# Kernel optimization log

Hardware: AMD Instinct MI355X
Metric: run time of the kernel (lower is better)

## Reference

```python
import jax, jax.numpy as jnp
import numpy as np

N_NODES = 100000
N_EDGES = 1600000
IN_DIM, HID_DIM, OUT_DIM = 128, 64, 64


def setup_inputs() -> dict:
    key = jax.random.key(0)
    ks = jax.random.split(key, 12)
    x = jax.random.normal(ks[0], (N_NODES, IN_DIM), dtype=jnp.float32)
    src = jax.random.randint(ks[1], (N_EDGES,), 0, N_NODES, dtype=jnp.int32)
    dst = jax.random.randint(ks[2], (N_EDGES,), 0, N_NODES, dtype=jnp.int32)
    def glorot(k, shape):
        lim = float(np.sqrt(6.0 / (shape[0] + shape[1])))
        return jax.random.uniform(k, shape, jnp.float32, -lim, lim)
    W0 = glorot(ks[3], (IN_DIM, HID_DIM)); b0 = jnp.zeros((HID_DIM,), jnp.float32)
    W1 = glorot(ks[4], (HID_DIM, HID_DIM)); b1 = jnp.zeros((HID_DIM,), jnp.float32)
    W2 = glorot(ks[5], (HID_DIM, OUT_DIM)); b2 = jnp.zeros((OUT_DIM,), jnp.float32)
    Wl = glorot(ks[6], (OUT_DIM, OUT_DIM)); bl = jnp.zeros((OUT_DIM,), jnp.float32)
    return {"x": x, "src": src, "dst": dst,
            "W0": W0, "b0": b0, "W1": W1, "b1": b1,
            "W2": W2, "b2": b2, "Wl": Wl, "bl": bl}


def _graph_conv(x, src, dst, W, b, inv_sqrt_out, inv_sqrt_in):
    # DGL GraphConv, norm='both': D_out^{-1/2} then XW, SpMM aggregate, D_in^{-1/2}, +bias
    h = x * inv_sqrt_out[:, None]          # [N, d_in]
    h = h @ W                               # [N, d_out] (project first: d_in >= d_out)
    agg = jax.ops.segment_sum(h[src], dst, num_segments=N_NODES)  # gather+scatter over edges
    return agg * inv_sqrt_in[:, None] + b


def reference(x, src, dst, W0, b0, W1, b1, W2, b2, Wl, bl):
    ones_e = jnp.ones((N_EDGES,), jnp.float32)
    deg_out = jnp.clip(jax.ops.segment_sum(ones_e, src, num_segments=N_NODES), 1.0)
    deg_in = jnp.clip(jax.ops.segment_sum(ones_e, dst, num_segments=N_NODES), 1.0)
    inv_out = jax.lax.rsqrt(deg_out)
    inv_in = jax.lax.rsqrt(deg_in)
    h = jax.nn.elu(_graph_conv(x, src, dst, W0, b0, inv_out, inv_in))
    h = jax.nn.elu(_graph_conv(h, src, dst, W1, b1, inv_out, inv_in))
    h = _graph_conv(h, src, dst, W2, b2, inv_out, inv_in)
    return jax.nn.elu(h) @ Wl + bl
```

## Files before the change

### kernel.cpp

```cpp
#include <hip/hip_runtime.h>
#include <hip/hip_fp16.h>
#include <cstdint>
#include <cstddef>


#define WG 256
static constexpr int NCHUNK = 512;
static constexpr int RW_SH  = 7;
static constexpr int RWID   = 1 << RW_SH;
static constexpr int BPRO   = 32000;
static constexpr int NRO    = 4;
static constexpr int NCO    = 64;

typedef _Float16 half8 __attribute__((ext_vector_type(8)));
typedef _Float16 half2v __attribute__((ext_vector_type(2)));
typedef float f32x4 __attribute__((ext_vector_type(4)));

__device__ __forceinline__ int block_scan_excl(int v, int tid, int* sd, int& total) {
  sd[tid] = v;
  __syncthreads();
  for (int off = 1; off < 256; off <<= 1) {
    int t = (tid >= off) ? sd[tid - off] : 0;
    __syncthreads();
    sd[tid] += t;
    __syncthreads();
  }
  int incl = sd[tid];
  total = sd[255];
  __syncthreads();
  return incl - v;
}

__global__ __launch_bounds__(WG) void setup1_kernel(const int* __restrict__ src,
                                                    const int* __restrict__ dst,
                                                    int* __restrict__ cntA,
                                                    int* __restrict__ slab,
                                                    const float* __restrict__ W0,
                                                    const float* __restrict__ W1,
                                                    const float* __restrict__ W2,
                                                    const float* __restrict__ Wl,
                                                    _Float16* __restrict__ T0,
                                                    _Float16* __restrict__ T1,
                                                    _Float16* __restrict__ T2,
                                                    _Float16* __restrict__ Tl,
                                                    int NR, int N, int E, int EPC, int EPCO) {
  __shared__ int smem[BPRO / 2];
  const int b = blockIdx.x, tid = threadIdx.x;

  if (b < NCHUNK) {
    int* cnt = smem;
    for (int i = tid; i < NR; i += WG) cnt[i] = 0;
    __syncthreads();
    const int base = b * EPC;
    const int nv4 = EPC >> 2;
    const int4* d4 = (const int4*)(dst + base);
    for (int i = tid; i < nv4; i += WG) {
      const int e = base + (i << 2);
      if (e + 3 < E) {
        const int4 v = d4[i];
        atomicAdd(&cnt[v.x >> RW_SH], 1);
        atomicAdd(&cnt[v.y >> RW_SH], 1);
        atomicAdd(&cnt[v.z >> RW_SH], 1);
        atomicAdd(&cnt[v.w >> RW_SH], 1);
      } else {
        for (int j = 0; j < 4; ++j) {
          const int ee = e + j;
          if (ee < E) atomicAdd(&cnt[dst[ee] >> RW_SH], 1);
        }
      }
    }
    __syncthreads();
    for (int i = tid; i < NR; i += WG) cntA[i * NCHUNK + b] = cnt[i];
    return;
  }

  if (b < NCHUNK + NRO * NCO) {
    int* h = smem;
    const int bb = b - NCHUNK;
    const int rr = bb / NCO, cc = bb % NCO;
    for (int i = tid; i < (BPRO >> 3); i += WG) ((int4*)h)[i] = make_int4(0, 0, 0, 0);
    __syncthreads();
    const int lo = rr * BPRO;
    const int base = cc * EPCO;
    const int nv4 = EPCO >> 2;
    const int4* s4 = (const int4*)(src + base);
    for (int i = tid; i < nv4; i += WG) {
      const int e = base + (i << 2);
      if (e + 3 < E) {
        const int4 v = s4[i];
        unsigned x;
        x = (unsigned)(v.x - lo); if (x < (unsigned)BPRO) atomicAdd((unsigned*)&h[x >> 1], 1u << ((x & 1) << 4));
        x = (unsigned)(v.y - lo); if (x < (unsigned)BPRO) atomicAdd((unsigned*)&h[x >> 1], 1u << ((x & 1) << 4));
        x = (unsigned)(v.z - lo); if (x < (unsigned)BPRO) atomicAdd((unsigned*)&h[x >> 1], 1u << ((x & 1) << 4));
        x = (unsigned)(v.w - lo); if (x < (unsigned)BPRO) atomicAdd((unsigned*)&h[x >> 1], 1u << ((x & 1) << 4));
      } else {
        for (int j = 0; j < 4; ++j) {
          const int ee = e + j;
          if (ee < E) {
            const unsigned x = (unsigned)(src[ee] - lo);
            if (x < (unsigned)BPRO) atomicAdd((unsigned*)&h[x >> 1], 1u << ((x & 1) << 4));
          }
        }
      }
    }
    __syncthreads();
    const int NW = N >> 1;
    const int wbase = lo >> 1;
    int* srow = slab + (size_t)cc * NW;
    for (int i = tid; i < (BPRO >> 3); i += WG) {
      const int wg = wbase + (i << 2);
      if (wg + 3 < NW) {
        ((int4*)(srow + wg))[0] = ((const int4*)h)[i];
      } else {
        for (int j = 0; j < 4; ++j)
          if (wg + j < NW) srow[wg + j] = h[(i << 2) + j];
      }
    }
    return;
  }

  const float* W; _Float16* T; int K;
  switch (b - (NCHUNK + NRO * NCO)) {
    case 0: W = W0; T = T0; K = 128; break;
    case 1: W = W1; T = T1; K = 64; break;
    case 2: W = W2; T = T2; K = 64; break;
    default: W = Wl; T = Tl; K = 64; break;
  }
  for (int i = tid; i < K * 64; i += WG) {
    const int k = i >> 6, c = i & 63;
    T[c * K + k] = (_Float16)W[i];
  }
}

__global__ __launch_bounds__(WG) void setup2_kernel(const int* __restrict__ cntA,
                                                    int* __restrict__ base_rel,
                                                    int* __restrict__ cntR,
                                                    const int* __restrict__ slab,
                                                    float* __restrict__ invo,
                                                    int NR, int N) {
  __shared__ int sd[256];
  const int b = blockIdx.x, tid = threadIdx.x;

  if (b < NR) {
    const int row = b * NCHUNK;
    int t0, t1;
    const int v0 = cntA[row + tid];
    const int e0 = block_scan_excl(v0, tid, sd, t0);
    base_rel[row + tid] = e0;
    const int v1 = cntA[row + 256 + tid];
    const int e1 = block_scan_excl(v1, tid, sd, t1);
    base_rel[row + 256 + tid] = t0 + e1;
    if (tid == 0) cntR[b] = t0 + t1;
    return;
  }

  const int NW = N >> 1;
  const int i = (b - NR) * WG + tid;
  if (i >= NW) return;
  unsigned s = 0;
#pragma unroll
  for (int c = 0; c < NCO; ++c) s += (unsigned)slab[(size_t)c * NW + i];
  int d0 = (int)(s & 0xffffu); if (d0 < 1) d0 = 1;
  int d1 = (int)(s >> 16);     if (d1 < 1) d1 = 1;
  *(float2*)(invo + 2 * i) = make_float2(rsqrtf((float)d0), rsqrtf((float)d1));
}

template <int K, bool F16IN>
__device__ __forceinline__ void gemm_conv_body(int bid, const void* __restrict__ inv_,
                                               const _Float16* __restrict__ WT,
                                               const float* __restrict__ invo,
                                               _Float16* __restrict__ hP, int N) {
  const int tid = threadIdx.x;
  const int w = tid >> 6, l = tid & 63;
  const int rowA = bid * 64 + w * 16 + (l & 15);
  const int ar = (rowA < N) ? rowA : (N - 1);
  const int g8 = (l >> 4) * 8;

  f32x4 acc[4];
#pragma unroll
  for (int t = 0; t < 4; ++t) acc[t] = (f32x4){0.f, 0.f, 0.f, 0.f};

#pragma unroll
  for (int s = 0; s < K / 32; ++s) {
    const int kb = s * 32 + g8;
    half8 a;
    if constexpr (F16IN) {
      a = *(const half8*)((const _Float16*)inv_ + (size_t)ar * K + kb);
    } else {
      const float* in = (const float*)inv_;
      const float4 f0 = *(const float4*)(in + (size_t)ar * K + kb);
      const float4 f1 = *(const float4*)(in + (size_t)ar * K + kb + 4);
      a[0] = (_Float16)f0.x; a[1] = (_Float16)f0.y; a[2] = (_Float16)f0.z; a[3] = (_Float16)f0.w;
      a[4] = (_Float16)f1.x; a[5] = (_Float16)f1.y; a[6] = (_Float16)f1.z; a[7] = (_Float16)f1.w;
    }
#pragma unroll
    for (int t = 0; t < 4; ++t) {
      const half8 b = *(const half8*)(WT + (size_t)(16 * t + (l & 15)) * K + kb);
      acc[t] = __builtin_amdgcn_mfma_f32_16x16x32_f16(a, b, acc[t], 0, 0, 0);
    }
  }

  const int rbase = bid * 64 + w * 16 + (l >> 4) * 4;
#pragma unroll
  for (int r = 0; r < 4; ++r) {
    const int row = rbase + r;
    if (row < N) {
      const float sc = invo[row];
#pragma unroll
      for (int t = 0; t < 4; ++t)
        hP[(size_t)row * 64 + 16 * t + (l & 15)] = (_Float16)(acc[t][r] * sc);
    }
  }
}

__global__ __launch_bounds__(WG) void range_gemm0_kernel(const int* __restrict__ cntR,
                                                         int* __restrict__ rangeStart,
                                                         int* __restrict__ rptr,
                                                         const float* __restrict__ x,
                                                         const _Float16* __restrict__ WT0,
                                                         const float* __restrict__ invo,
                                                         _Float16* __restrict__ hP,
                                                         int NR, int N, int E) {
  __shared__ int sd[256];
  const int b = blockIdx.x, tid = threadIdx.x;
  if (b == 0) {
    int carry = 0;
    for (int base = 0; base < NR; base += 256) {
      const int idx = base + tid;
      const int v = (idx < NR) ? cntR[idx] : 0;
      int tot;
      const int e = block_scan_excl(v, tid, sd, tot);
      if (idx < NR) rangeStart[idx] = carry + e;
      carry += tot;
    }
    if (tid == 0) { rangeStart[NR] = E; rptr[N] = E; }
    return;
  }
  gemm_conv_body<128, false>(b - 1, x, WT0, invo, hP, N);
}

__global__ __launch_bounds__(WG) void bucket_kernel(const int* __restrict__ src,
                                                    const int* __restrict__ dst,
                                                    const int* __restrict__ base_rel,
                                                    const int* __restrict__ rangeStart,
                                                    int* __restrict__ bucket,
                                                    int NR, int E, int EPC) {
  __shared__ int cur[1024];
  const int c = blockIdx.x, tid = threadIdx.x;
  for (int i = tid; i < NR; i += WG) cur[i] = rangeStart[i] + base_rel[i * NCHUNK + c];
  __syncthreads();
  const int base = c * EPC;
  const int nv4 = EPC >> 2;
  const int4* s4 = (const int4*)(src + base);
  const int4* d4 = (const int4*)(dst + base);
  for (int i = tid; i < nv4; i += WG) {
    const int e = base + (i << 2);
    if (e + 3 < E) {
      const int4 sv = s4[i];
      const int4 dv = d4[i];
      int p;
      p = atomicAdd(&cur[dv.x >> RW_SH], 1); bucket[p] = (sv.x << RW_SH) | (dv.x & (RWID - 1));
      p = atomicAdd(&cur[dv.y >> RW_SH], 1); bucket[p] = (sv.y << RW_SH) | (dv.y & (RWID - 1));
      p = atomicAdd(&cur[dv.z >> RW_SH], 1); bucket[p] = (sv.z << RW_SH) | (dv.z & (RWID - 1));
      p = atomicAdd(&cur[dv.w >> RW_SH], 1); bucket[p] = (sv.w << RW_SH) | (dv.w & (RWID - 1));
    } else {
      for (int j = 0; j < 4; ++j) {
        const int ee = e + j;
        if (ee < E) {
          const int s = src[ee], d = dst[ee];
          const int p = atomicAdd(&cur[d >> RW_SH], 1);
          bucket[p] = (s << RW_SH) | (d & (RWID - 1));
        }
      }
    }
  }
}

__global__ __launch_bounds__(WG) void csr_kernel(const int* __restrict__ bucket,
                                                 const int* __restrict__ rangeStart,
                                                 int* __restrict__ rptr,
                                                 float* __restrict__ invi,
                                                 int* __restrict__ esrc, int N) {
  __shared__ int hist[RWID], sd[256];
  const int r = blockIdx.x, tid = threadIdx.x;
  const int s0 = rangeStart[r], s1 = rangeStart[r + 1];
  if (tid < RWID) hist[tid] = 0;
  __syncthreads();
  for (int e = s0 + tid; e < s1; e += WG) atomicAdd(&hist[bucket[e] & (RWID - 1)], 1);
  __syncthreads();
  const int v = (tid < RWID) ? hist[tid] : 0;
  int tot;
  const int excl = block_scan_excl(v, tid, sd, tot);
  const int node = (r << RW_SH) + tid;
  if (tid < RWID && node < N) {
    rptr[node] = s0 + excl;
    invi[node] = rsqrtf((float)((v < 1) ? 1 : v));
  }
  if (tid < RWID) hist[tid] = s0 + excl;
  __syncthreads();
  for (int e = s0 + tid; e < s1; e += WG) {
    const int pk = bucket[e];
    const int p = atomicAdd(&hist[pk & (RWID - 1)], 1);
    esrc[p] = pk >> RW_SH;
  }
}

template <int K, bool F16IN>
__global__ __launch_bounds__(256) void gemm_conv_mfma(const void* __restrict__ inv_,
                                                      const _Float16* __restrict__ WT,
                                                      const float* __restrict__ invo,
                                                      _Float16* __restrict__ hP, int N) {
  gemm_conv_body<K, F16IN>(blockIdx.x, inv_, WT, invo, hP, N);
}

__global__ __launch_bounds__(256) void gemm_head_mfma(const _Float16* __restrict__ in,
                                                      const _Float16* __restrict__ WT,
                                                      const float* __restrict__ bias,
                                                      float* __restrict__ out, int N) {
  constexpr int K = 64;
  const int tid = threadIdx.x;
  const int w = tid >> 6, l = tid & 63;
  const int rowA = blockIdx.x * 64 + w * 16 + (l & 15);
  const int ar = (rowA < N) ? rowA : (N - 1);
  const int g8 = (l >> 4) * 8;

  f32x4 acc[4];
#pragma unroll
  for (int t = 0; t < 4; ++t) acc[t] = (f32x4){0.f, 0.f, 0.f, 0.f};

#pragma unroll
  for (int s = 0; s < K / 32; ++s) {
    const int kb = s * 32 + g8;
    const half8 a = *(const half8*)(in + (size_t)ar * K + kb);
#pragma unroll
    for (int t = 0; t < 4; ++t) {
      const half8 b = *(const half8*)(WT + (size_t)(16 * t + (l & 15)) * K + kb);
      acc[t] = __builtin_amdgcn_mfma_f32_16x16x32_f16(a, b, acc[t], 0, 0, 0);
    }
  }

  const int rbase = blockIdx.x * 64 + w * 16 + (l >> 4) * 4;
#pragma unroll
  for (int r = 0; r < 4; ++r) {
    const int row = rbase + r;
    if (row < N) {
#pragma unroll
      for (int t = 0; t < 4; ++t) {
        const int c = 16 * t + (l & 15);
        out[(size_t)row * 64 + c] = acc[t][r] + bias[c];
      }
    }
  }
}

__global__ __launch_bounds__(256) void agg_kernel(const _Float16* __restrict__ hp,
                                                  const int* __restrict__ rptr,
                                                  const int* __restrict__ esrc,
                                                  const float* __restrict__ invin,
                                                  const float* __restrict__ bias,
                                                  _Float16* __restrict__ out, int N,
                                                  int apply_elu) {
  const int w = (blockIdx.x * 256 + threadIdx.x) >> 6;
  const int lane = threadIdx.x & 63;
  const int g = lane >> 3;
  const int f8 = lane & 7;
  if (w >= N) return;
  const int e0 = rptr[w];
  const int e1 = rptr[w + 1];
  const int f = f8 * 8 + g;
  const float vi = invin[w];
  const float bv = bias[f];

  float acc[8];
#pragma unroll
  for (int k = 0; k < 8; ++k) acc[k] = 0.f;

  int e = e0;
  for (; e + 16 <= e1; e += 16) {
    const int sA = esrc[e + g];
    const int sB = esrc[e + 8 + g];
    const half8 hA8 = *(const half8*)(hp + (size_t)sA * 64 + f8 * 8);
    const half8 hB8 = *(const half8*)(hp + (size_t)sB * 64 + f8 * 8);
#if __has_builtin(__builtin_amdgcn_fdot2)
    const half2v one2 = {(_Float16)1.0f, (_Float16)1.0f};
#pragma unroll
    for (int k = 0; k < 8; ++k) {
      half2v p; p[0] = hA8[k]; p[1] = hB8[k];
      acc[k] = __builtin_amdgcn_fdot2(p, one2, acc[k], false);
    }
#else
#pragma unroll
    for (int k = 0; k < 8; ++k) acc[k] += (float)hA8[k] + (float)hB8[k];
#endif
  }
  for (; e + 8 <= e1; e += 8) {
    const int s = esrc[e + g];
    const half8 hv = *(const half8*)(hp + (size_t)s * 64 + f8 * 8);
#pragma unroll
    for (int k = 0; k < 8; ++k) acc[k] += (float)hv[k];
  }
  if (e < e1) {
    const int rem = e1 - e;
    int idx = e + g; if (idx > e1 - 1) idx = e1 - 1;
    const int s = esrc[idx];
    const half8 hv = *(const half8*)(hp + (size_t)s * 64 + f8 * 8);
    const float m = (g < rem) ? 1.f : 0.f;
#pragma unroll
    for (int k = 0; k < 8; ++k) acc[k] = fmaf(m, (float)hv[k], acc[k]);
  }

  const bool gb0 = (g & 1) != 0;
  const float s0 = gb0 ? acc[0] : acc[1];
  const float s1 = gb0 ? acc[2] : acc[3];
  const float s2 = gb0 ? acc[4] : acc[5];
  const float s3 = gb0 ? acc[6] : acc[7];
  const float k0 = (gb0 ? acc[1] : acc[0]) + __shfl_xor(s0, 8);
  const float k1 = (gb0 ? acc[3] : acc[2]) + __shfl_xor(s1, 8);
  const float k2 = (gb0 ? acc[5] : acc[4]) + __shfl_xor(s2, 8);
  const float k3 = (gb0 ? acc[7] : acc[6]) + __shfl_xor(s3, 8);
  const bool gb1 = (g & 2) != 0;
  const float t0 = gb1 ? k0 : k1;
  const float t1 = gb1 ? k2 : k3;
  const float m0 = (gb1 ? k1 : k0) + __shfl_xor(t0, 16);
  const float m1 = (gb1 ? k3 : k2) + __shfl_xor(t1, 16);
  const bool gb2 = (g & 4) != 0;
  const float u0 = gb2 ? m0 : m1;
  float v = (gb2 ? m1 : m0) + __shfl_xor(u0, 32);

  v = v * vi + bv;
  if (apply_elu) v = (v > 0.f) ? v : (__expf(v) - 1.0f);
  out[(size_t)w * 64 + f] = (_Float16)v;
}

extern "C" void kernel_launch(void* const* d_in, const int* in_sizes, int n_in,
                              void* d_out, int out_size, void* d_ws, size_t ws_size,
                              hipStream_t stream) {
  const float* x  = (const float*)d_in[0];
  const int*   src = (const int*)d_in[1];
  const int*   dst = (const int*)d_in[2];
  const float* W0 = (const float*)d_in[3];
  const float* b0 = (const float*)d_in[4];
  const float* W1 = (const float*)d_in[5];
  const float* b1 = (const float*)d_in[6];
  const float* W2 = (const float*)d_in[7];
  const float* b2 = (const float*)d_in[8];
  const float* Wl = (const float*)d_in[9];
  const float* bl = (const float*)d_in[10];

  const int N = in_sizes[0] / 128;
  const int E = in_sizes[1];
  const int NR = (N + RWID - 1) >> RW_SH;
  const int EPC = (((E + NCHUNK - 1) / NCHUNK) + 3) & ~3;
  const int EPCO = (((E + NCO - 1) / NCO) + 3) & ~3;

  int* wsp = (int*)d_ws;
  size_t off = 0;
  auto alloc = [&](size_t n) -> int* {
    int* p = wsp + off;
    off += (n + 63) & ~(size_t)63;
    return p;
  };
  float*    invo       = (float*)alloc(N);
  float*    invi       = (float*)alloc(N);
  int*      rptr       = alloc((size_t)N + 1);
  int*      esrc       = alloc(E);
  int*      cntA       = alloc((size_t)NR * NCHUNK);
  int*      base_rel   = alloc((size_t)NR * NCHUNK);
  int*      cntR       = alloc(NR);
  int*      rangeStart = alloc((size_t)NR + 1);
  int*      bucket     = alloc(E);
  int*      slab       = alloc((size_t)NCO * (N >> 1));
  _Float16* hP         = (_Float16*)alloc((size_t)N * 32);
  _Float16* hA         = (_Float16*)alloc((size_t)N * 32);
  _Float16* WT0        = (_Float16*)alloc(64 * 128 / 2);
  _Float16* WT1        = (_Float16*)alloc(64 * 64 / 2);
  _Float16* WT2        = (_Float16*)alloc(64 * 64 / 2);
  _Float16* WTl        = (_Float16*)alloc(64 * 64 / 2);
  (void)ws_size; (void)n_in; (void)out_size;

  const int gAgg = (N + 3) / 4;
  const int gGemm = (N + 63) / 64;
  const int gInvo = ((N >> 1) + WG - 1) / WG;

  setup1_kernel<<<NCHUNK + NRO * NCO + 4, WG, 0, stream>>>(
      src, dst, cntA, slab, W0, W1, W2, Wl, WT0, WT1, WT2, WTl, NR, N, E, EPC, EPCO);
  setup2_kernel<<<NR + gInvo, WG, 0, stream>>>(cntA, base_rel, cntR, slab, invo, NR, N);
  range_gemm0_kernel<<<1 + gGemm, WG, 0, stream>>>(cntR, rangeStart, rptr, x, WT0, invo, hP, NR, N, E);
  bucket_kernel<<<NCHUNK, WG, 0, stream>>>(src, dst, base_rel, rangeStart, bucket, NR, E, EPC);
  csr_kernel<<<NR, WG, 0, stream>>>(bucket, rangeStart, rptr, invi, esrc, N);

  agg_kernel<<<gAgg, 256, 0, stream>>>(hP, rptr, esrc, invi, b0, hA, N, 1);
  gemm_conv_mfma<64, true><<<gGemm, 256, 0, stream>>>(hA, WT1, invo, hP, N);
  agg_kernel<<<gAgg, 256, 0, stream>>>(hP, rptr, esrc, invi, b1, hA, N, 1);
  gemm_conv_mfma<64, true><<<gGemm, 256, 0, stream>>>(hA, WT2, invo, hP, N);
  agg_kernel<<<gAgg, 256, 0, stream>>>(hP, rptr, esrc, invi, b2, hA, N, 1);
  gemm_head_mfma<<<gGemm, 256, 0, stream>>>(hA, WTl, bl, (float*)d_out, N);
}
```

Baseline: 240.8 us.

## Fold range scan into setup2 via last-block ticket; merge bucket with gemm0

Moves the global exclusive scan over per-range counts into setup2, where the last block to finish (found with an atomic ticket reset in setup1) runs it. The bucket scatter and the first-layer GEMM now share one launch. This removes one kernel launch and its dependency barrier, and lets the scatter and the GEMM run at the same time. The cost is an extra threadfence plus atomic in every setup2 block and a serial scan in a single tail block.

```diff
diff --git a/kernel.cpp b/kernel.cpp
--- a/kernel.cpp
+++ b/kernel.cpp
@@ -43,6 +43,7 @@
                                                     _Float16* __restrict__ T1,
                                                     _Float16* __restrict__ T2,
                                                     _Float16* __restrict__ Tl,
+                                                    int* __restrict__ ticket,
                                                     int NR, int N, int E, int EPC, int EPCO) {
   __shared__ int smem[BPRO / 2];
   const int b = blockIdx.x, tid = threadIdx.x;
@@ -119,8 +120,10 @@
     return;
   }
 
+  const int wb = b - (NCHUNK + NRO * NCO);
+  if (wb == 0 && tid == 0) *ticket = 0;
   const float* W; _Float16* T; int K;
-  switch (b - (NCHUNK + NRO * NCO)) {
+  switch (wb) {
     case 0: W = W0; T = T0; K = 128; break;
     case 1: W = W1; T = T1; K = 64; break;
     case 2: W = W2; T = T2; K = 64; break;
@@ -137,8 +140,12 @@
                                                     int* __restrict__ cntR,
                                                     const int* __restrict__ slab,
                                                     float* __restrict__ invo,
-                                                    int NR, int N) {
+                                                    int* __restrict__ ticket,
+                                                    int* __restrict__ rangeStart,
+                                                    int* __restrict__ rptr,
+                                                    int NR, int N, int E) {
   __shared__ int sd[256];
+  __shared__ int isLast;
   const int b = blockIdx.x, tid = threadIdx.x;
 
   if (b < NR) {
@@ -151,18 +158,39 @@
     const int e1 = block_scan_excl(v1, tid, sd, t1);
     base_rel[row + 256 + tid] = t0 + e1;
     if (tid == 0) cntR[b] = t0 + t1;
-    return;
-  }
-
-  const int NW = N >> 1;
-  const int i = (b - NR) * WG + tid;
-  if (i >= NW) return;
-  unsigned s = 0;
-#pragma unroll
-  for (int c = 0; c < NCO; ++c) s += (unsigned)slab[(size_t)c * NW + i];
-  int d0 = (int)(s & 0xffffu); if (d0 < 1) d0 = 1;
-  int d1 = (int)(s >> 16);     if (d1 < 1) d1 = 1;
-  *(float2*)(invo + 2 * i) = make_float2(rsqrtf((float)d0), rsqrtf((float)d1));
+  } else {
+    const int NW = N >> 1;
+    const int i = (b - NR) * WG + tid;
+    if (i < NW) {
+      unsigned s = 0;
+#pragma unroll
+      for (int c = 0; c < NCO; ++c) s += (unsigned)slab[(size_t)c * NW + i];
+      int d0 = (int)(s & 0xffffu); if (d0 < 1) d0 = 1;
+      int d1 = (int)(s >> 16);     if (d1 < 1) d1 = 1;
+      *(float2*)(invo + 2 * i) = make_float2(rsqrtf((float)d0), rsqrtf((float)d1));
+    }
+  }
+
+  __syncthreads();
+  __threadfence();
+  if (tid == 0) {
+    const int t = atomicAdd(ticket, 1);
+    isLast = (t == (int)gridDim.x - 1) ? 1 : 0;
+  }
+  __syncthreads();
+  if (isLast) {
+    __threadfence();
+    int carry = 0;
+    for (int base = 0; base < NR; base += 256) {
+      const int idx = base + tid;
+      const int v = (idx < NR) ? cntR[idx] : 0;
+      int tot;
+      const int e = block_scan_excl(v, tid, sd, tot);
+      if (idx < NR) rangeStart[idx] = carry + e;
+      carry += tot;
+    }
+    if (tid == 0) { rangeStart[NR] = E; rptr[N] = E; }
+  }
 }
 
 template <int K, bool F16IN>
@@ -213,40 +241,25 @@
   }
 }
 
-__global__ __launch_bounds__(WG) void range_gemm0_kernel(const int* __restrict__ cntR,
-                                                         int* __restrict__ rangeStart,
-                                                         int* __restrict__ rptr,
-                                                         const float* __restrict__ x,
-                                                         const _Float16* __restrict__ WT0,
-                                                         const float* __restrict__ invo,
-                                                         _Float16* __restrict__ hP,
-                                                         int NR, int N, int E) {
-  __shared__ int sd[256];
+__global__ __launch_bounds__(WG) void bucket_gemm0_kernel(const int* __restrict__ src,
+                                                          const int* __restrict__ dst,
+                                                          const int* __restrict__ base_rel,
+                                                          const int* __restrict__ rangeStart,
+                                                          int* __restrict__ bucket,
+                                                          const float* __restrict__ x,
+                                                          const _Float16* __restrict__ WT0,
+                                                          const float* __restrict__ invo,
+                                                          _Float16* __restrict__ hP,
+                                                          int NR, int N, int E, int EPC) {
+  __shared__ int cur[1024];
   const int b = blockIdx.x, tid = threadIdx.x;
-  if (b == 0) {
-    int carry = 0;
-    for (int base = 0; base < NR; base += 256) {
-      const int idx = base + tid;
-      const int v = (idx < NR) ? cntR[idx] : 0;
-      int tot;
-      const int e = block_scan_excl(v, tid, sd, tot);
-      if (idx < NR) rangeStart[idx] = carry + e;
-      carry += tot;
-    }
-    if (tid == 0) { rangeStart[NR] = E; rptr[N] = E; }
+
+  if (b >= NCHUNK) {
+    gemm_conv_body<128, false>(b - NCHUNK, x, WT0, invo, hP, N);
     return;
   }
-  gemm_conv_body<128, false>(b - 1, x, WT0, invo, hP, N);
-}
-
-__global__ __launch_bounds__(WG) void bucket_kernel(const int* __restrict__ src,
-                                                    const int* __restrict__ dst,
-                                                    const int* __restrict__ base_rel,
-                                                    const int* __restrict__ rangeStart,
-                                                    int* __restrict__ bucket,
-                                                    int NR, int E, int EPC) {
-  __shared__ int cur[1024];
-  const int c = blockIdx.x, tid = threadIdx.x;
+
+  const int c = b;
   for (int i = tid; i < NR; i += WG) cur[i] = rangeStart[i] + base_rel[i * NCHUNK + c];
   __syncthreads();
   const int base = c * EPC;
@@ -470,6 +483,7 @@
   int*      rangeStart = alloc((size_t)NR + 1);
   int*      bucket     = alloc(E);
   int*      slab       = alloc((size_t)NCO * (N >> 1));
+  int*      ticket     = alloc(64);
   _Float16* hP         = (_Float16*)alloc((size_t)N * 32);
   _Float16* hA         = (_Float16*)alloc((size_t)N * 32);
   _Float16* WT0        = (_Float16*)alloc(64 * 128 / 2);
@@ -483,10 +497,11 @@
   const int gInvo = ((N >> 1) + WG - 1) / WG;
 
   setup1_kernel<<<NCHUNK + NRO * NCO + 4, WG, 0, stream>>>(
-      src, dst, cntA, slab, W0, W1, W2, Wl, WT0, WT1, WT2, WTl, NR, N, E, EPC, EPCO);
-  setup2_kernel<<<NR + gInvo, WG, 0, stream>>>(cntA, base_rel, cntR, slab, invo, NR, N);
-  range_gemm0_kernel<<<1 + gGemm, WG, 0, stream>>>(cntR, rangeStart, rptr, x, WT0, invo, hP, NR, N, E);
-  bucket_kernel<<<NCHUNK, WG, 0, stream>>>(src, dst, base_rel, rangeStart, bucket, NR, E, EPC);
+      src, dst, cntA, slab, W0, W1, W2, Wl, WT0, WT1, WT2, WTl, ticket, NR, N, E, EPC, EPCO);
+  setup2_kernel<<<NR + gInvo, WG, 0, stream>>>(cntA, base_rel, cntR, slab, invo,
+                                               ticket, rangeStart, rptr, NR, N, E);
+  bucket_gemm0_kernel<<<NCHUNK + gGemm, WG, 0, stream>>>(
+      src, dst, base_rel, rangeStart, bucket, x, WT0, invo, hP, NR, N, E, EPC);
   csr_kernel<<<NR, WG, 0, stream>>>(bucket, rangeStart, rptr, invi, esrc, N);
 
   agg_kernel<<<gAgg, 256, 0, stream>>>(hP, rptr, esrc, invi, b0, hA, N, 1);
```

Measured after the change: 304.6 us. +26.5%, slower.
